# Performance work log

Hardware: AMD Instinct MI355X
Metric: run time of the kernel (lower is better)

## Reference

```python
import jax, jax.numpy as jnp
import numpy as np

V, E, H, B, S, T = 32000, 32, 128, 128, 512, 16


def _gru_cell(x, h, w_ih, w_hh, b_ih, b_hh):
    # PyTorch GRU cell semantics.  x: [B, in], h: [B, H]
    gi = x @ w_ih.T + b_ih              # [B, 3H]
    gh = h @ w_hh.T + b_hh              # [B, 3H]
    i_r, i_z, i_n = jnp.split(gi, 3, axis=-1)
    h_r, h_z, h_n = jnp.split(gh, 3, axis=-1)
    r = jax.nn.sigmoid(i_r + h_r)
    z = jax.nn.sigmoid(i_z + h_z)
    n = jnp.tanh(i_n + r * h_n)
    return (1.0 - z) * n + z * h


def setup_inputs() -> dict:
    key = jax.random.key(0)
    ks = jax.random.split(key, 24)
    Hh = H // 2  # encoder hidden per direction = 64
    u = lambda k, shp, fan: jax.random.uniform(k, shp, jnp.float32, -1.0, 1.0) / np.sqrt(fan)
    inp = {
        'inputs': jax.random.randint(ks[0], (B, S), 0, V),
        'targets': jax.random.randint(ks[1], (B, T), 0, V),
        'emb': jax.random.normal(ks[2], (V, E), jnp.float32),
        # encoder forward direction
        'W_ih_f': u(ks[3], (3 * Hh, E), Hh), 'W_hh_f': u(ks[4], (3 * Hh, Hh), Hh),
        'b_ih_f': u(ks[5], (3 * Hh,), Hh), 'b_hh_f': u(ks[6], (3 * Hh,), Hh),
        # encoder backward direction
        'W_ih_b': u(ks[7], (3 * Hh, E), Hh), 'W_hh_b': u(ks[8], (3 * Hh, Hh), Hh),
        'b_ih_b': u(ks[9], (3 * Hh,), Hh), 'b_hh_b': u(ks[10], (3 * Hh,), Hh),
        # sGate linears
        'W1': u(ks[11], (H, H), H), 'b1': u(ks[12], (H,), H),
        'W2': u(ks[13], (H, H), H), 'b2': u(ks[14], (H,), H),
        # decoder GRU (input E + H = 160, hidden H)
        'W_ih_d': u(ks[15], (3 * H, E + H), H), 'W_hh_d': u(ks[16], (3 * H, H), H),
        'b_ih_d': u(ks[17], (3 * H,), H), 'b_hh_d': u(ks[18], (3 * H,), H),
        # decoder2vocab
        'W_out': u(ks[19], (V, H), H), 'b_out': u(ks[20], (V,), H),
    }
    return inp


def reference(inputs, targets, emb, W_ih_f, W_hh_f, b_ih_f, b_hh_f,
              W_ih_b, W_hh_b, b_ih_b, b_hh_b, W1, b1, W2, b2,
              W_ih_d, W_hh_d, b_ih_d, b_hh_d, W_out, b_out):
    Hh = H // 2
    # ---- encode ----
    embeds = emb[inputs]                       # [B, S, E]
    xs = embeds.transpose(1, 0, 2)             # [S, B, E] time-major
    h0 = jnp.zeros((inputs.shape[0], Hh), jnp.float32)

    def fwd_step(h, x):
        h = _gru_cell(x, h, W_ih_f, W_hh_f, b_ih_f, b_hh_f)
        return h, h

    def bwd_step(h, x):
        h = _gru_cell(x, h, W_ih_b, W_hh_b, b_ih_b, b_hh_b)
        return h, h

    h_f, outs_f = jax.lax.scan(fwd_step, h0, xs)
    h_b, outs_b = jax.lax.scan(bwd_step, h0, xs[::-1])
    outs_b = outs_b[::-1]
    outputs = jnp.concatenate([outs_f, outs_b], axis=-1).transpose(1, 0, 2)  # [B, S, H]
    sn = jnp.concatenate([h_f, h_b], axis=-1)[:, None, :]                    # [B, 1, H]
    sGate = jax.nn.sigmoid(outputs @ W1.T + b1 + sn @ W2.T + b2)
    enc_outs = outputs * sGate                                               # [B, S, H]

    # ---- attention decode (teacher forcing) ----
    h_dec0 = sn[:, 0, :]                       # [B, H]
    words = targets[:, :-1].T                  # [T-1, B]

    def dec_step(h, w):
        e = emb[w]                                                  # [B, E]
        alpha = jax.nn.softmax(jnp.einsum('bd,bsd->bs', h, enc_outs))
        c_t = jnp.einsum('bs,bsd->bd', alpha, enc_outs)             # [B, H]
        h = _gru_cell(jnp.concatenate([c_t, e], axis=-1), h,
                      W_ih_d, W_hh_d, b_ih_d, b_hh_d)
        return h, h @ W_out.T + b_out

    _, logits = jax.lax.scan(dec_step, h_dec0, words)  # [T-1, B, V]
    return logits.transpose(1, 0, 2)                   # [B, T-1, V]
```

## Files before the change

kernel.cpp:

```cpp
#include <hip/hip_runtime.h>
#include <hip/hip_bf16.h>


typedef unsigned short u16;
typedef unsigned int u32;
typedef __attribute__((ext_vector_type(8))) short short8;
typedef __attribute__((ext_vector_type(4))) float f32x4;

#define V_ 32000
#define E_ 32
#define H_ 128
#define B_ 128
#define S_ 512
#define TDEC 15

__device__ __forceinline__ float bfu(u32 u) {
    union { u32 i; float f; } v; v.i = u << 16; return v.f;
}
__device__ __forceinline__ u16 f2bf(float f) {
    union { float f; u32 i; } v; v.f = f;
    u32 x = v.i;
    u32 r = (x + 0x7fffu + ((x >> 16) & 1u)) >> 16;
    return (u16)r;
}
__device__ __forceinline__ void bf8_to_f(const uint4 p, float* f) {
    f[0] = bfu(p.x & 0xffffu); f[1] = bfu(p.x >> 16);
    f[2] = bfu(p.y & 0xffffu); f[3] = bfu(p.y >> 16);
    f[4] = bfu(p.z & 0xffffu); f[5] = bfu(p.z >> 16);
    f[6] = bfu(p.w & 0xffffu); f[7] = bfu(p.w >> 16);
}
__device__ __forceinline__ float sigm(float x) { return 1.f / (1.f + expf(-x)); }
__device__ __forceinline__ float sigm_fast(float x) { return 1.f / (1.f + __expf(-x)); }
__device__ __forceinline__ float tanh_fast(float x) {
    const float t = __expf(2.f * x);
    return (t - 1.f) / (t + 1.f);
}

__global__ __launch_bounds__(384) void gi_kernel(
    const int* __restrict__ inputs, const float* __restrict__ emb,
    const float* __restrict__ Wih_f, const float* __restrict__ bih_f,
    const float* __restrict__ bhh_f,
    const float* __restrict__ Wih_b, const float* __restrict__ bih_b,
    const float* __restrict__ bhh_b,
    float* __restrict__ gi)
{
    const int b  = blockIdx.x >> 3;
    const int s0 = (blockIdx.x & 7) << 6;
    const int tid = threadIdx.x;

    __shared__ float xs[64][E_];
    __shared__ int idx[64];
    if (tid < 64) idx[tid] = inputs[b * S_ + s0 + tid];
    __syncthreads();
    for (int i = tid; i < 64 * E_; i += 384) {
        xs[i >> 5][i & 31] = emb[(unsigned)idx[i >> 5] * E_ + (i & 31)];
    }
    __syncthreads();

    const int dir = (tid >= 192) ? 1 : 0;
    const int j = tid - dir * 192;
    const float* Wih = dir ? Wih_b : Wih_f;
    const float* bih = dir ? bih_b : bih_f;
    const float* bhh = dir ? bhh_b : bhh_f;

    float w[E_];
    #pragma unroll
    for (int k = 0; k < E_; k += 4)
        *(float4*)(w + k) = *(const float4*)(Wih + j * E_ + k);
    const float c = bih[j] + (j < 128 ? bhh[j] : 0.f);

    float* gout = gi + (((size_t)(dir * B_ + b)) * S_ + s0) * 192 + j;
    for (int r = 0; r < 64; r++) {
        const float4* xr = (const float4*)xs[r];
        float a0 = 0.f, a1 = 0.f, a2 = 0.f, a3 = 0.f;
        #pragma unroll
        for (int q = 0; q < E_ / 4; q++) {
            const float4 x = xr[q];
            a0 += x.x * w[4 * q + 0]; a1 += x.y * w[4 * q + 1];
            a2 += x.z * w[4 * q + 2]; a3 += x.w * w[4 * q + 3];
        }
        gout[(size_t)r * 192] = ((a0 + a1) + (a2 + a3)) + c;
    }
}

__global__ __launch_bounds__(192, 1) void encoder_kernel(
    const float* __restrict__ gi,
    const float* __restrict__ Whh_f, const float* __restrict__ bhh_f,
    const float* __restrict__ Whh_b, const float* __restrict__ bhh_b,
    u16* __restrict__ outputs, float* __restrict__ sn)
{
    const int tid = threadIdx.x;
    const int g = tid >> 6;
    const int j = tid & 63;
    const int b = blockIdx.x & 127;
    const int dir = blockIdx.x >> 7;

    const float* Whh = dir ? Whh_b : Whh_f;
    const float* bhh = dir ? bhh_b : bhh_f;

    f32x4 wv[16];
    {
        const f32x4* wr = (const f32x4*)(Whh + (g * 64 + j) * 64);
        #pragma unroll
        for (int k = 0; k < 16; k++) wv[k] = wr[k];
    }
    const float badd = (g == 2) ? bhh[128 + j] : 0.f;

    __shared__ __attribute__((aligned(16))) float hs[64];
    __shared__ float sg[4 * 64];
    if (tid < 64) hs[tid] = 0.f;
    float hmine = 0.f;

    const float* gp = gi + ((size_t)(dir * B_ + b)) * S_ * 192 + g * 64 + j;
    u16* orow = outputs + ((size_t)b * S_) * H_ + (dir << 6) + j;

    const int st = dir ? -1 : 1;
    int oc = dir ? (S_ - 1) : 0;

    float pa = gp[(long)oc * 192];
    float pb = gp[(long)(oc + st) * 192];

#define ENC_STEP(PCUR)                                                         \
    {                                                                          \
        __syncthreads();                  \
        f32x4 acc = {0.f, 0.f, 0.f, 0.f};                                      \
        _Pragma("unroll")                                                      \
        for (int q = 0; q < 16; q++)                                           \
            acc += *(const f32x4*)(hs + 4 * q) * wv[q];                        \
        const float d = (acc[0] + acc[1]) + (acc[2] + acc[3]);                 \
        if (g == 2) { sg[128 + j] = d + badd; sg[192 + j] = PCUR; }            \
        else        { sg[g * 64 + j] = d + PCUR; }                             \
        PCUR = gp[(long)(oc + 2 * st) * 192];           \
        __syncthreads();                                         \
        if (g == 0) {                                                          \
            const float r = sigm_fast(sg[j]);                                  \
            const float z = sigm_fast(sg[64 + j]);                             \
            const float n = tanh_fast(sg[192 + j] + r * sg[128 + j]);          \
            const float hn = n + z * (hmine - n);                              \
            hmine = hn;                                                        \
            hs[j] = hn;                                                        \
            orow[(long)oc * H_] = f2bf(hn);                                    \
        }                                                                      \
        oc += st;                                                              \
    }

    for (int s = 0; s < S_; s += 2) {
        ENC_STEP(pa)
        ENC_STEP(pb)
    }
#undef ENC_STEP

    if (g == 0) sn[(b << 7) + (dir << 6) + j] = hmine;
}

__global__ __launch_bounds__(128) void t2_kernel(
    const float* __restrict__ sn, const float* __restrict__ W2,
    const float* __restrict__ b2, float* __restrict__ t2)
{
    const int b = blockIdx.x, h = threadIdx.x;
    __shared__ float s_[H_];
    s_[h] = sn[b * H_ + h];
    __syncthreads();
    const float4* wr = (const float4*)(W2 + h * H_);
    float a0 = 0.f, a1 = 0.f, a2 = 0.f, a3 = 0.f;
    #pragma unroll 4
    for (int k = 0; k < H_ / 4; k++) {
        const float4 p = wr[k];
        a0 += s_[4 * k + 0] * p.x; a1 += s_[4 * k + 1] * p.y;
        a2 += s_[4 * k + 2] * p.z; a3 += s_[4 * k + 3] * p.w;
    }
    t2[b * H_ + h] = ((a0 + a1) + (a2 + a3)) + b2[h];
}

__global__ __launch_bounds__(256) void cvt_bf16_kernel(
    const float* __restrict__ src, u16* __restrict__ dst)
{
    const int i = (blockIdx.x * 256 + threadIdx.x) * 4;
    const float4 p = *(const float4*)(src + i);
    ushort4 q;
    q.x = f2bf(p.x); q.y = f2bf(p.y); q.z = f2bf(p.z); q.w = f2bf(p.w);
    *(ushort4*)(dst + i) = q;
}

__global__ __launch_bounds__(256) void gate_mfma_kernel(
    const u16* __restrict__ outputs, const u16* __restrict__ W1b,
    const float* __restrict__ b1, const float* __restrict__ t2,
    u16* __restrict__ enc)
{
    const int l = threadIdx.x & 63;
    const int w = threadIdx.x >> 6;
    const int tile_m = blockIdx.x * 64 + w * 16;
    const int row_a = tile_m + (l & 15);
    const int kb = (l >> 4) * 8;
    const int b = blockIdx.x >> 3;

    f32x4 acc[8] = {};
    #pragma unroll
    for (int kk = 0; kk < 4; kk++) {
        const int k0 = kk * 32 + kb;
        const short8 af = *(const short8*)(outputs + row_a * H_ + k0);
        #pragma unroll
        for (int i = 0; i < 8; i++) {
            const int n = i * 16 + (l & 15);
            const short8 bv = *(const short8*)(W1b + n * H_ + k0);
            acc[i] = __builtin_amdgcn_mfma_f32_16x16x32_bf16(af, bv, acc[i], 0, 0, 0);
        }
    }

    const int m_base = tile_m + (l >> 4) * 4;
    #pragma unroll
    for (int i = 0; i < 8; i++) {
        const int n = i * 16 + (l & 15);
        const float bias = b1[n] + t2[b * H_ + n];
        #pragma unroll
        for (int r = 0; r < 4; r++) {
            const int m = m_base + r;
            const float g = sigm_fast(acc[i][r] + bias);
            const float o = bfu(outputs[m * H_ + n]);
            enc[m * H_ + n] = f2bf(o * g);
        }
    }
}

__global__ __launch_bounds__(256) void decoder_kernel(
    const int* __restrict__ targets, const float* __restrict__ emb,
    const float* __restrict__ Wihd, const float* __restrict__ Whhd,
    const float* __restrict__ bihd, const float* __restrict__ bhhd,
    const u16* __restrict__ enc, const float* __restrict__ sn,
    u16* __restrict__ h_all)
{
    const int b = blockIdx.x;
    const int tid = threadIdx.x;
    __shared__ float h[H_];
    __shared__ float sc[S_];
    __shared__ float xv[H_ + E_];
    __shared__ float red[256];
    __shared__ float chalf[2][H_];
    __shared__ float sgi[3 * H_];
    __shared__ float sgh[3 * H_];

    if (tid < H_) h[tid] = sn[b * H_ + tid];
    __syncthreads();

    const u16* encb = enc + b * S_ * H_;

    for (int t = 0; t < TDEC; t++) {
        const int word = targets[b * 16 + t];

        for (int s = tid; s < S_; s += 256) {
            const u16* row = encb + s * H_;
            float a0 = 0.f, a1 = 0.f, a2 = 0.f, a3 = 0.f;
            for (int k = 0; k < H_; k += 8) {
                uint4 p = *(const uint4*)(row + k);
                float f[8]; bf8_to_f(p, f);
                a0 += h[k + 0] * f[0]; a1 += h[k + 1] * f[1];
                a2 += h[k + 2] * f[2]; a3 += h[k + 3] * f[3];
                a0 += h[k + 4] * f[4]; a1 += h[k + 5] * f[5];
                a2 += h[k + 6] * f[6]; a3 += h[k + 7] * f[7];
            }
            sc[s] = (a0 + a1) + (a2 + a3);
        }
        __syncthreads();

        red[tid] = fmaxf(sc[tid], sc[tid + 256]);
        __syncthreads();
        for (int off = 128; off > 0; off >>= 1) {
            if (tid < off) red[tid] = fmaxf(red[tid], red[tid + off]);
            __syncthreads();
        }
        const float m = red[0];
        __syncthreads();
        const float e0 = expf(sc[tid] - m);
        const float e1 = expf(sc[tid + 256] - m);
        red[tid] = e0 + e1;
        __syncthreads();
        for (int off = 128; off > 0; off >>= 1) {
            if (tid < off) red[tid] = red[tid] + red[tid + off];
            __syncthreads();
        }
        const float inv = 1.f / red[0];
        __syncthreads();
        sc[tid] = e0 * inv;
        sc[tid + 256] = e1 * inv;
        __syncthreads();

        {
            const int k = tid & 127;
            const int half = tid >> 7;
            const u16* basep = encb + (half * 256) * H_ + k;
            const float* al = sc + half * 256;
            float c0 = 0.f, c1 = 0.f, c2 = 0.f, c3 = 0.f;
            for (int s = 0; s < 256; s += 4) {
                c0 += al[s + 0] * bfu(basep[(s + 0) * H_]);
                c1 += al[s + 1] * bfu(basep[(s + 1) * H_]);
                c2 += al[s + 2] * bfu(basep[(s + 2) * H_]);
                c3 += al[s + 3] * bfu(basep[(s + 3) * H_]);
            }
            chalf[half][k] = (c0 + c1) + (c2 + c3);
        }
        __syncthreads();
        if (tid < H_) xv[tid] = chalf[0][tid] + chalf[1][tid];
        else if (tid < H_ + E_) xv[tid] = emb[(unsigned)word * E_ + (tid - H_)];
        __syncthreads();

        for (int j = tid; j < 3 * H_; j += 256) {
            const float4* wr = (const float4*)(Wihd + j * (H_ + E_));
            float a0 = 0.f, a1 = 0.f, a2 = 0.f, a3 = 0.f;
            for (int k = 0; k < (H_ + E_) / 4; k++) {
                const float4 p = wr[k];
                a0 += xv[4 * k + 0] * p.x; a1 += xv[4 * k + 1] * p.y;
                a2 += xv[4 * k + 2] * p.z; a3 += xv[4 * k + 3] * p.w;
            }
            sgi[j] = ((a0 + a1) + (a2 + a3)) + bihd[j];

            const float4* hr = (const float4*)(Whhd + j * H_);
            float b0 = 0.f, b1_ = 0.f, b2_ = 0.f, b3 = 0.f;
            for (int k = 0; k < H_ / 4; k++) {
                const float4 p = hr[k];
                b0  += h[4 * k + 0] * p.x; b1_ += h[4 * k + 1] * p.y;
                b2_ += h[4 * k + 2] * p.z; b3  += h[4 * k + 3] * p.w;
            }
            sgh[j] = ((b0 + b1_) + (b2_ + b3)) + bhhd[j];
        }
        __syncthreads();

        if (tid < H_) {
            const float r = sigm(sgi[tid] + sgh[tid]);
            const float z = sigm(sgi[H_ + tid] + sgh[H_ + tid]);
            const float n = tanhf(sgi[2 * H_ + tid] + r * sgh[2 * H_ + tid]);
            const float hn = (1.f - z) * n + z * h[tid];
            h[tid] = hn;
            h_all[(t * B_ + b) * H_ + tid] = f2bf(hn);
        }
        __syncthreads();
    }
}

__global__ __launch_bounds__(256) void logits_kernel(
    const u16* __restrict__ hall, const u16* __restrict__ Woutb,
    const float* __restrict__ bout, float* __restrict__ out)
{
    const int l = threadIdx.x & 63;
    const int w = threadIdx.x >> 6;
    const int tile_n = blockIdx.x * 64;
    const int tile_m = blockIdx.y * 64 + w * 16;

    f32x4 acc[4] = {};
    const int row_a = tile_m + (l & 15);
    const int kb = (l >> 4) * 8;

    #pragma unroll
    for (int kk = 0; kk < 4; kk++) {
        const int k0 = kk * 32 + kb;
        const short8 af = *(const short8*)(hall + row_a * H_ + k0);
        #pragma unroll
        for (int i = 0; i < 4; i++) {
            const int n = tile_n + i * 16 + (l & 15);
            const short8 bv = *(const short8*)(Woutb + n * H_ + k0);
            acc[i] = __builtin_amdgcn_mfma_f32_16x16x32_bf16(af, bv, acc[i], 0, 0, 0);
        }
    }

    const int m_base = tile_m + (l >> 4) * 4;
    #pragma unroll
    for (int i = 0; i < 4; i++) {
        const int n = tile_n + i * 16 + (l & 15);
        const float bias = bout[n];
        #pragma unroll
        for (int r = 0; r < 4; r++) {
            const int m = m_base + r;
            const int t = m >> 7;
            const int bb = m & 127;
            out[(size_t)(bb * TDEC + t) * V_ + n] = acc[i][r] + bias;
        }
    }
}

extern "C" void kernel_launch(void* const* d_in, const int* in_sizes, int n_in,
                              void* d_out, int out_size, void* d_ws, size_t ws_size,
                              hipStream_t stream) {
    const int*   inputs  = (const int*)d_in[0];
    const int*   targets = (const int*)d_in[1];
    const float* emb     = (const float*)d_in[2];
    const float* Wih_f   = (const float*)d_in[3];
    const float* Whh_f   = (const float*)d_in[4];
    const float* bih_f   = (const float*)d_in[5];
    const float* bhh_f   = (const float*)d_in[6];
    const float* Wih_b   = (const float*)d_in[7];
    const float* Whh_b   = (const float*)d_in[8];
    const float* bih_b   = (const float*)d_in[9];
    const float* bhh_b   = (const float*)d_in[10];
    const float* W1      = (const float*)d_in[11];
    const float* b1      = (const float*)d_in[12];
    const float* W2      = (const float*)d_in[13];
    const float* b2      = (const float*)d_in[14];
    const float* Wihd    = (const float*)d_in[15];
    const float* Whhd    = (const float*)d_in[16];
    const float* bihd    = (const float*)d_in[17];
    const float* bhhd    = (const float*)d_in[18];
    const float* Wout    = (const float*)d_in[19];
    const float* bout    = (const float*)d_in[20];
    float* out = (float*)d_out;

    u16*   outputs = (u16*)d_out;
    u16*   enc     = (u16*)((char*)d_out + 16777216);
    u16*   W1b     = (u16*)((char*)d_out + 33554432);
    float* gi      = (float*)((char*)d_out + 33619968);

    char* ws = (char*)d_ws;
    float* sn    = (float*)(ws);
    float* t2    = (float*)(ws + 65536);
    u16*   h_all = (u16*)(ws + 131072);
    u16*   Woutb = (u16*)(ws + 622592);

    gi_kernel<<<B_ * (S_ / 64), 384, 0, stream>>>(inputs, emb, Wih_f, bih_f, bhh_f,
                                                  Wih_b, bih_b, bhh_b, gi);
    encoder_kernel<<<256, 192, 0, stream>>>(gi, Whh_f, bhh_f, Whh_b, bhh_b, outputs, sn);
    t2_kernel<<<128, 128, 0, stream>>>(sn, W2, b2, t2);
    cvt_bf16_kernel<<<H_ * H_ / 1024, 256, 0, stream>>>(W1, W1b);
    cvt_bf16_kernel<<<V_ * H_ / 1024, 256, 0, stream>>>(Wout, Woutb);
    gate_mfma_kernel<<<B_ * S_ / 64, 256, 0, stream>>>(outputs, W1b, b1, t2, enc);
    decoder_kernel<<<128, 256, 0, stream>>>(targets, emb, Wihd, Whhd, bihd, bhhd,
                                            enc, sn, h_all);
    logits_kernel<<<dim3(500, 30), 256, 0, stream>>>(h_all, Woutb, bout, out);
}
```

Measured before the change: 1.042 ms.

## Widen decoder blocks to 512 threads with wave-shuffle softmax reductions

The decoder kernel now runs 512 threads per batch row, so each thread scores one encoder position and the context sum is split four ways instead of two. The tree reductions through shared memory, each step behind a block barrier, are replaced by wavefront shuffle reductions plus a small per-wave combine. Hidden-state reads become vectorized and several loops are unrolled. The aim is to shorten the serial per-step latency of the 128-block decoder, at the cost of more threads per block that may sit idle in the GRU gate phase.

```diff
diff --git a/kernel.cpp b/kernel.cpp
--- a/kernel.cpp
+++ b/kernel.cpp
@@ -222,7 +222,7 @@
     }
 }
 
-__global__ __launch_bounds__(256) void decoder_kernel(
+__global__ __launch_bounds__(512) void decoder_kernel(
     const int* __restrict__ targets, const float* __restrict__ emb,
     const float* __restrict__ Wihd, const float* __restrict__ Whhd,
     const float* __restrict__ bihd, const float* __restrict__ bhhd,
@@ -231,11 +231,14 @@
 {
     const int b = blockIdx.x;
     const int tid = threadIdx.x;
-    __shared__ float h[H_];
+    const int lane = tid & 63;
+    const int wid = tid >> 6;
+
+    __shared__ __attribute__((aligned(16))) float h[H_];
     __shared__ float sc[S_];
     __shared__ float xv[H_ + E_];
-    __shared__ float red[256];
-    __shared__ float chalf[2][H_];
+    __shared__ float redm[8], reds[8];
+    __shared__ float cpart[4][H_];
     __shared__ float sgi[3 * H_];
     __shared__ float sgh[3 * H_];
 
@@ -247,74 +250,76 @@
     for (int t = 0; t < TDEC; t++) {
         const int word = targets[b * 16 + t];
 
-        for (int s = tid; s < S_; s += 256) {
-            const u16* row = encb + s * H_;
-            float a0 = 0.f, a1 = 0.f, a2 = 0.f, a3 = 0.f;
-            for (int k = 0; k < H_; k += 8) {
-                uint4 p = *(const uint4*)(row + k);
-                float f[8]; bf8_to_f(p, f);
-                a0 += h[k + 0] * f[0]; a1 += h[k + 1] * f[1];
-                a2 += h[k + 2] * f[2]; a3 += h[k + 3] * f[3];
-                a0 += h[k + 4] * f[4]; a1 += h[k + 5] * f[5];
-                a2 += h[k + 6] * f[6]; a3 += h[k + 7] * f[7];
-            }
-            sc[s] = (a0 + a1) + (a2 + a3);
-        }
-        __syncthreads();
-
-        red[tid] = fmaxf(sc[tid], sc[tid + 256]);
-        __syncthreads();
-        for (int off = 128; off > 0; off >>= 1) {
-            if (tid < off) red[tid] = fmaxf(red[tid], red[tid + off]);
-            __syncthreads();
-        }
-        const float m = red[0];
-        __syncthreads();
-        const float e0 = expf(sc[tid] - m);
-        const float e1 = expf(sc[tid + 256] - m);
-        red[tid] = e0 + e1;
-        __syncthreads();
-        for (int off = 128; off > 0; off >>= 1) {
-            if (tid < off) red[tid] = red[tid] + red[tid + off];
-            __syncthreads();
-        }
-        const float inv = 1.f / red[0];
-        __syncthreads();
-        sc[tid] = e0 * inv;
-        sc[tid + 256] = e1 * inv;
+        const u16* row = encb + tid * H_;
+        float a0 = 0.f, a1 = 0.f, a2 = 0.f, a3 = 0.f;
+        #pragma unroll
+        for (int k = 0; k < H_; k += 8) {
+            uint4 p = *(const uint4*)(row + k);
+            float f[8]; bf8_to_f(p, f);
+            const f32x4 h0 = *(const f32x4*)(h + k);
+            const f32x4 h1 = *(const f32x4*)(h + k + 4);
+            a0 += h0[0] * f[0]; a1 += h0[1] * f[1];
+            a2 += h0[2] * f[2]; a3 += h0[3] * f[3];
+            a0 += h1[0] * f[4]; a1 += h1[1] * f[5];
+            a2 += h1[2] * f[6]; a3 += h1[3] * f[7];
+        }
+        const float d = (a0 + a1) + (a2 + a3);
+
+        float m = d;
+        #pragma unroll
+        for (int off = 32; off > 0; off >>= 1) m = fmaxf(m, __shfl_xor(m, off));
+        if (lane == 0) redm[wid] = m;
+        __syncthreads();
+        float bm = redm[0];
+        #pragma unroll
+        for (int i = 1; i < 8; i++) bm = fmaxf(bm, redm[i]);
+        const float e = expf(d - bm);
+        float ssum = e;
+        #pragma unroll
+        for (int off = 32; off > 0; off >>= 1) ssum += __shfl_xor(ssum, off);
+        if (lane == 0) reds[wid] = ssum;
+        __syncthreads();
+        float tot = reds[0];
+        #pragma unroll
+        for (int i = 1; i < 8; i++) tot += reds[i];
+        sc[tid] = e * (1.f / tot);
         __syncthreads();
 
         {
             const int k = tid & 127;
-            const int half = tid >> 7;
-            const u16* basep = encb + (half * 256) * H_ + k;
-            const float* al = sc + half * 256;
+            const int q = tid >> 7;
+            const u16* basep = encb + (q * 128) * H_ + k;
+            const float* al = sc + q * 128;
             float c0 = 0.f, c1 = 0.f, c2 = 0.f, c3 = 0.f;
-            for (int s = 0; s < 256; s += 4) {
+            #pragma unroll 8
+            for (int s = 0; s < 128; s += 4) {
                 c0 += al[s + 0] * bfu(basep[(s + 0) * H_]);
                 c1 += al[s + 1] * bfu(basep[(s + 1) * H_]);
                 c2 += al[s + 2] * bfu(basep[(s + 2) * H_]);
                 c3 += al[s + 3] * bfu(basep[(s + 3) * H_]);
             }
-            chalf[half][k] = (c0 + c1) + (c2 + c3);
-        }
-        __syncthreads();
-        if (tid < H_) xv[tid] = chalf[0][tid] + chalf[1][tid];
+            cpart[q][k] = (c0 + c1) + (c2 + c3);
+        }
+        __syncthreads();
+        if (tid < H_) xv[tid] = (cpart[0][tid] + cpart[1][tid]) + (cpart[2][tid] + cpart[3][tid]);
         else if (tid < H_ + E_) xv[tid] = emb[(unsigned)word * E_ + (tid - H_)];
         __syncthreads();
 
-        for (int j = tid; j < 3 * H_; j += 256) {
+        if (tid < 3 * H_) {
+            const int j = tid;
             const float4* wr = (const float4*)(Wihd + j * (H_ + E_));
-            float a0 = 0.f, a1 = 0.f, a2 = 0.f, a3 = 0.f;
+            float g0 = 0.f, g1 = 0.f, g2 = 0.f, g3 = 0.f;
+            #pragma unroll 8
             for (int k = 0; k < (H_ + E_) / 4; k++) {
                 const float4 p = wr[k];
-                a0 += xv[4 * k + 0] * p.x; a1 += xv[4 * k + 1] * p.y;
-                a2 += xv[4 * k + 2] * p.z; a3 += xv[4 * k + 3] * p.w;
+                g0 += xv[4 * k + 0] * p.x; g1 += xv[4 * k + 1] * p.y;
+                g2 += xv[4 * k + 2] * p.z; g3 += xv[4 * k + 3] * p.w;
             }
-            sgi[j] = ((a0 + a1) + (a2 + a3)) + bihd[j];
+            sgi[j] = ((g0 + g1) + (g2 + g3)) + bihd[j];
 
             const float4* hr = (const float4*)(Whhd + j * H_);
             float b0 = 0.f, b1_ = 0.f, b2_ = 0.f, b3 = 0.f;
+            #pragma unroll 8
             for (int k = 0; k < H_ / 4; k++) {
                 const float4 p = hr[k];
                 b0  += h[4 * k + 0] * p.x; b1_ += h[4 * k + 1] * p.y;
@@ -420,7 +425,7 @@
     cvt_bf16_kernel<<<H_ * H_ / 1024, 256, 0, stream>>>(W1, W1b);
     cvt_bf16_kernel<<<V_ * H_ / 1024, 256, 0, stream>>>(Wout, Woutb);
     gate_mfma_kernel<<<B_ * S_ / 64, 256, 0, stream>>>(outputs, W1b, b1, t2, enc);
-    decoder_kernel<<<128, 256, 0, stream>>>(targets, emb, Wihd, Whhd, bihd, bhhd,
+    decoder_kernel<<<128, 512, 0, stream>>>(targets, emb, Wihd, Whhd, bihd, bhhd,
                                             enc, sn, h_all);
     logits_kernel<<<dim3(500, 30), 256, 0, stream>>>(h_all, Woutb, bout, out);
 }
```

After: 972.0 us. 1.07x faster.
